# Kernel optimization log

Hardware: AMD Instinct MI355X
Metric: run time of the kernel (lower is better)

Reference implementation:

```python
import jax, jax.numpy as jnp
import numpy as np

NUM_ITEMS = 50000
EMB = 16
SLATE = 10
HID = 512
LAT = 64
RESP = 1024
BATCH = 256


def _linear_params(k, out_dim, in_dim):
    kw, kb = jax.random.split(k)
    s = 1.0 / np.sqrt(in_dim)
    W = jax.random.uniform(kw, (out_dim, in_dim), jnp.float32, -s, s)
    b = jax.random.uniform(kb, (out_dim,), jnp.float32, -s, s)
    return W, b


def setup_inputs() -> dict:
    key = jax.random.key(0)
    ks = jax.random.split(key, 10)
    user_repr = jax.random.randint(ks[0], (BATCH, NUM_ITEMS), 0, 2, dtype=jnp.int32)
    slate = jax.random.randint(ks[1], (BATCH, SLATE), 0, NUM_ITEMS, dtype=jnp.int32)
    response_encoded = jax.random.uniform(ks[2], (BATCH, RESP), jnp.float32)
    eps = jax.random.normal(ks[3], (BATCH, LAT), jnp.float32)
    emb = jax.random.normal(ks[4], (NUM_ITEMS, EMB), jnp.float32)
    in_enc = SLATE * EMB + EMB + RESP
    W_enc, b_enc = _linear_params(ks[5], HID, in_enc)
    W_mu, b_mu = _linear_params(ks[6], LAT, HID)
    W_lv, b_lv = _linear_params(ks[7], LAT, HID)
    in_dec = LAT + EMB + RESP
    W_d1, b_d1 = _linear_params(ks[8], HID, in_dec)
    W_d2, b_d2 = _linear_params(ks[9], SLATE * EMB, HID)
    return {"user_repr": user_repr, "slate": slate, "response_encoded": response_encoded,
            "eps": eps, "emb": emb, "W_enc": W_enc, "b_enc": b_enc,
            "W_mu": W_mu, "b_mu": b_mu, "W_lv": W_lv, "b_lv": b_lv,
            "W_d1": W_d1, "b_d1": b_d1, "W_d2": W_d2, "b_d2": b_d2}


def reference(user_repr, slate, response_encoded, eps, emb,
              W_enc, b_enc, W_mu, b_mu, W_lv, b_lv, W_d1, b_d1, W_d2, b_d2):
    # Ragged embedding-mean pooling over interacted items (vectorized segment mean):
    # mean of emb rows where user_repr==1  ==  (indicator @ emb) / count
    uf = user_repr.astype(jnp.float32)                       # [B, N]
    counts = jnp.sum(uf, axis=1, keepdims=True)              # [B, 1]
    user = (uf @ emb) / counts                               # [B, E]

    cond = jnp.concatenate([user, response_encoded], axis=1)  # [B, E+R]
    slate_emb = emb[slate]                                    # [B, K, E]
    slate_vec = slate_emb.reshape(-1, SLATE * EMB)            # [B, K*E]
    x = jnp.concatenate([slate_vec, cond], axis=1)

    # encoder
    h = jax.nn.relu(x @ W_enc.T + b_enc)
    z_mean = h @ W_mu.T + b_mu
    z_log_var = h @ W_lv.T + b_lv

    # reparameterized sample
    z = z_mean + eps * jnp.exp(0.5 * z_log_var)

    # decoder
    dz = jnp.concatenate([z, cond], axis=1)
    dh = jax.nn.relu(dz @ W_d1.T + b_d1)
    rx = jax.nn.relu(dh @ W_d2.T + b_d2)                      # [B, K*E]
    rx = rx.reshape(-1, SLATE, EMB)                           # [B, K, E]

    # scores vs all items, softmax over items
    logits = jnp.einsum('bkh,nh->bkn', rx, emb)               # [B, K, N]
    probs = jax.nn.softmax(logits, axis=2)
    recon_slate = jnp.argmax(probs, axis=2)                   # [B, K]
    recon_resp = jnp.take_along_axis(probs, slate[:, :, None], axis=2)[..., 0]  # [B, K]
    return z_mean, z_log_var, recon_slate, recon_resp
```

## Files before the change

### kernel.cpp

```cpp
#include <hip/hip_runtime.h>

#define NITEMS 50000
#define EMBD   16
#define NSLATE 10
#define HIDD   512
#define LATD   64
#define RESPD  1024
#define BATCH  256
#define NCHUNK 8
#define CHUNK  6250
#define PCHUNK 3125
#define LOG2E  1.44269504088896340736f
#define SHIFT  64.0f

#define OUT_ZM 0
#define OUT_ZLV 16384
#define OUT_RS 32768
#define OUT_RR 35328

#define WS_X    0
#define WS_DZ   307200
#define WS_P2   0
#define WS_PP   589824
#define WS_PART 589824
#define WS_RX   1114112
#define WS_SPS  1155072
#define WS_SPM  1175552
#define WS_SPA  1196032

__global__ __launch_bounds__(256) void pool_part(const int* __restrict__ u,
    const float* __restrict__ emb, float* __restrict__ pp) {
  int b = blockIdx.x, c = blockIdx.y, t = threadIdx.x;
  float acc[16];
  #pragma unroll
  for (int i = 0; i < 16; ++i) acc[i] = 0.0f;
  float cnt = 0.0f;
  const int* ub = u + (size_t)b * NITEMS;
  int n1 = c * PCHUNK + PCHUNK;
  for (int n = c * PCHUNK + t; n < n1; n += 256) {
    if (ub[n]) {
      const float4* e4 = (const float4*)(emb + (size_t)n * 16);
      float4 a = e4[0], bb = e4[1], cc = e4[2], dd = e4[3];
      acc[0] += a.x;  acc[1] += a.y;  acc[2] += a.z;  acc[3] += a.w;
      acc[4] += bb.x; acc[5] += bb.y; acc[6] += bb.z; acc[7] += bb.w;
      acc[8] += cc.x; acc[9] += cc.y; acc[10] += cc.z; acc[11] += cc.w;
      acc[12] += dd.x; acc[13] += dd.y; acc[14] += dd.z; acc[15] += dd.w;
      cnt += 1.0f;
    }
  }
  #pragma unroll
  for (int off = 32; off > 0; off >>= 1) {
    #pragma unroll
    for (int i = 0; i < 16; ++i) acc[i] += __shfl_down(acc[i], off);
    cnt += __shfl_down(cnt, off);
  }
  int lane = t & 63, wv = t >> 6;
  if (lane == 0) {
    float* dst = pp + ((size_t)(b * 16 + c) * 4 + wv) * 17;
    #pragma unroll
    for (int i = 0; i < 16; ++i) dst[i] = acc[i];
    dst[16] = cnt;
  }
}

__global__ __launch_bounds__(256) void build_x(const float* __restrict__ pp,
    const int* __restrict__ slate, const float* __restrict__ resp,
    const float* __restrict__ emb, float* __restrict__ x, float* __restrict__ dz) {
  __shared__ float fin[17];
  int b = blockIdx.x, t = threadIdx.x;
  if (t < 17) {
    float a = 0.f;
    const float* p = pp + (size_t)b * 64 * 17 + t;
    #pragma unroll
    for (int w = 0; w < 64; ++w) a += p[w * 17];
    fin[t] = a;
  }
  __syncthreads();
  float inv = 1.0f / fin[16];
  if (t < 16) {
    float uv = fin[t] * inv;
    x[b * 1200 + 160 + t] = uv;
    dz[b * 1104 + 64 + t] = uv;
  }
  if (t >= 32 && t < 192) {
    int i = t - 32;
    int k = i >> 4, e = i & 15;
    int it = slate[b * 10 + k];
    x[b * 1200 + i] = emb[(size_t)it * 16 + e];
  }
  for (int i = t; i < 1024; i += 256) {
    float r = resp[b * 1024 + i];
    x[b * 1200 + 176 + i] = r;
    dz[b * 1104 + 80 + i] = r;
  }
}

__global__ __launch_bounds__(256) void gemm64(const float* __restrict__ A,
    const float* __restrict__ B, float* __restrict__ P, int M, int N, int K, int kChunk) {
  __shared__ float As[16][68];
  __shared__ float Bs[16][68];
  int tid = threadIdx.x;
  int m0 = blockIdx.y * 64, n0 = blockIdx.x * 64;
  int ks = blockIdx.z * kChunk;
  int ke = ks + kChunk; if (ke > K) ke = K;
  int sr = tid >> 2;
  int sc = (tid & 3) * 4;
  int tx = tid & 15, ty = tid >> 4;
  float acc[4][4];
  #pragma unroll
  for (int i = 0; i < 4; ++i)
    #pragma unroll
    for (int j = 0; j < 4; ++j) acc[i][j] = 0.f;
  for (int k0 = ks; k0 < ke; k0 += 16) {
    float4 av = make_float4(0.f, 0.f, 0.f, 0.f);
    float4 bv = make_float4(0.f, 0.f, 0.f, 0.f);
    if (k0 + sc < ke)
      av = *(const float4*)(A + (size_t)(m0 + sr) * K + k0 + sc);
    if (k0 + sc < ke && n0 + sr < N)
      bv = *(const float4*)(B + (size_t)(n0 + sr) * K + k0 + sc);
    __syncthreads();
    As[sc][sr] = av.x; As[sc + 1][sr] = av.y; As[sc + 2][sr] = av.z; As[sc + 3][sr] = av.w;
    Bs[sc][sr] = bv.x; Bs[sc + 1][sr] = bv.y; Bs[sc + 2][sr] = bv.z; Bs[sc + 3][sr] = bv.w;
    __syncthreads();
    #pragma unroll
    for (int kk = 0; kk < 16; ++kk) {
      float4 a4 = *(const float4*)&As[kk][4 * ty];
      float4 b4 = *(const float4*)&Bs[kk][4 * tx];
      float a[4] = {a4.x, a4.y, a4.z, a4.w};
      float b[4] = {b4.x, b4.y, b4.z, b4.w};
      #pragma unroll
      for (int i = 0; i < 4; ++i)
        #pragma unroll
        for (int j = 0; j < 4; ++j) acc[i][j] = fmaf(a[i], b[j], acc[i][j]);
    }
  }
  float* Pz = P + (size_t)blockIdx.z * M * N;
  #pragma unroll
  for (int i = 0; i < 4; ++i) {
    int m = m0 + 4 * ty + i, n = n0 + 4 * tx;
    if (n < N)
      *(float4*)(Pz + (size_t)m * N + n) = make_float4(acc[i][0], acc[i][1], acc[i][2], acc[i][3]);
  }
}

__global__ __launch_bounds__(128) void mulv_z_kernel(const float* __restrict__ part,
    const float* __restrict__ benc,
    const float* __restrict__ Wmu, const float* __restrict__ bmu,
    const float* __restrict__ Wlv, const float* __restrict__ blv,
    const float* __restrict__ eps, float* __restrict__ out, float* __restrict__ dz) {
  __shared__ __align__(16) float hs[512];
  __shared__ float zms[64], zlvs[64];
  int b = blockIdx.x, t = threadIdx.x;
  for (int i = t; i < 512; i += 128) {
    float a = benc[i];
    #pragma unroll
    for (int s = 0; s < 4; ++s) a += part[(size_t)s * 131072 + b * 512 + i];
    hs[i] = fmaxf(a, 0.f);
  }
  __syncthreads();
  const float* Wr = (t < 64) ? (Wmu + (size_t)t * 512) : (Wlv + (size_t)(t - 64) * 512);
  float bias = (t < 64) ? bmu[t] : blv[t - 64];
  const float4* w4 = (const float4*)Wr;
  const float4* h4 = (const float4*)hs;
  float a0 = 0.f, a1 = 0.f, a2 = 0.f, a3 = 0.f;
  #pragma unroll 4
  for (int i = 0; i < 128; ++i) {
    float4 w = w4[i], hv = h4[i];
    a0 = fmaf(w.x, hv.x, a0); a1 = fmaf(w.y, hv.y, a1);
    a2 = fmaf(w.z, hv.z, a2); a3 = fmaf(w.w, hv.w, a3);
  }
  float acc = (a0 + a1) + (a2 + a3) + bias;
  if (t < 64) { out[OUT_ZM + b * 64 + t] = acc; zms[t] = acc; }
  else        { out[OUT_ZLV + b * 64 + (t - 64)] = acc; zlvs[t - 64] = acc; }
  __syncthreads();
  if (t < 64) {
    float zv = fmaf(eps[b * 64 + t], __builtin_amdgcn_exp2f(0.7213475204444817f * zlvs[t]), zms[t]);
    dz[b * 1104 + t] = zv;
  }
}

__global__ __launch_bounds__(256) void gemm_d2(const float* __restrict__ part,
    const float* __restrict__ bd1, const float* __restrict__ W, float* __restrict__ p2) {
  __shared__ float As[16][68];
  __shared__ float Bs[16][68];
  const int N = 160;
  int tid = threadIdx.x;
  int m0 = blockIdx.y * 64, n0 = blockIdx.x * 64;
  int ks = blockIdx.z * 64, ke = ks + 64;
  int sr = tid >> 2, sc = (tid & 3) * 4;
  int tx = tid & 15, ty = tid >> 4;
  float acc[4][4];
  #pragma unroll
  for (int i = 0; i < 4; ++i)
    #pragma unroll
    for (int j = 0; j < 4; ++j) acc[i][j] = 0.f;
  for (int k0 = ks; k0 < ke; k0 += 16) {
    int col = k0 + sc;
    const float* p = part + (size_t)(m0 + sr) * 512 + col;
    float4 a0 = *(const float4*)(p);
    float4 a1 = *(const float4*)(p + 131072);
    float4 a2 = *(const float4*)(p + 262144);
    float4 a3 = *(const float4*)(p + 393216);
    float4 bb = *(const float4*)(bd1 + col);
    float4 av;
    av.x = fmaxf(a0.x + a1.x + a2.x + a3.x + bb.x, 0.f);
    av.y = fmaxf(a0.y + a1.y + a2.y + a3.y + bb.y, 0.f);
    av.z = fmaxf(a0.z + a1.z + a2.z + a3.z + bb.z, 0.f);
    av.w = fmaxf(a0.w + a1.w + a2.w + a3.w + bb.w, 0.f);
    float4 bv = make_float4(0.f, 0.f, 0.f, 0.f);
    if (n0 + sr < N)
      bv = *(const float4*)(W + (size_t)(n0 + sr) * 512 + col);
    __syncthreads();
    As[sc][sr] = av.x; As[sc + 1][sr] = av.y; As[sc + 2][sr] = av.z; As[sc + 3][sr] = av.w;
    Bs[sc][sr] = bv.x; Bs[sc + 1][sr] = bv.y; Bs[sc + 2][sr] = bv.z; Bs[sc + 3][sr] = bv.w;
    __syncthreads();
    #pragma unroll
    for (int kk = 0; kk < 16; ++kk) {
      float4 a4 = *(const float4*)&As[kk][4 * ty];
      float4 b4 = *(const float4*)&Bs[kk][4 * tx];
      float a[4] = {a4.x, a4.y, a4.z, a4.w};
      float b[4] = {b4.x, b4.y, b4.z, b4.w};
      #pragma unroll
      for (int i = 0; i < 4; ++i)
        #pragma unroll
        for (int j = 0; j < 4; ++j) acc[i][j] = fmaf(a[i], b[j], acc[i][j]);
    }
  }
  float* Pz = p2 + (size_t)blockIdx.z * 40960;
  #pragma unroll
  for (int i = 0; i < 4; ++i) {
    int m = m0 + 4 * ty + i, n = n0 + 4 * tx;
    if (n < N)
      *(float4*)(Pz + (size_t)m * 160 + n) = make_float4(acc[i][0], acc[i][1], acc[i][2], acc[i][3]);
  }
}

__global__ __launch_bounds__(256, 2) void score_part(const float* __restrict__ p2,
    const float* __restrict__ bd2, const float* __restrict__ emb,
    float* __restrict__ rx, float* __restrict__ psg, float* __restrict__ pmg,
    int* __restrict__ pag) {
  __shared__ __align__(16) float rxs[160];
  __shared__ float wm[4][10], wsum[4][10];
  __shared__ int wa[4][10];
  int b = blockIdx.x, c = blockIdx.y, t = threadIdx.x;
  if (t < 160) {
    float a = bd2[t];
    #pragma unroll
    for (int z = 0; z < 8; ++z) a += p2[(size_t)z * 40960 + b * 160 + t];
    float v = fmaxf(a, 0.f) * LOG2E;
    rxs[t] = v;
    if (c == 0) rx[b * 160 + t] = v;
  }
  __syncthreads();
  float m[10], s[10];
  int am[10];
  #pragma unroll
  for (int k = 0; k < 10; ++k) { m[k] = -3.402823466e38f; s[k] = 0.f; am[k] = 0; }
  int nBase = c * CHUNK;
  const float4* ep = (const float4*)emb;
  #pragma unroll 1
  for (int j = 0; j < 12; ++j) {
    int n0 = nBase + j * 512 + t;
    float4 e[2][4];
    #pragma unroll
    for (int it = 0; it < 2; ++it) {
      const float4* p = ep + (size_t)(n0 + it * 256) * 4;
      e[it][0] = p[0]; e[it][1] = p[1]; e[it][2] = p[2]; e[it][3] = p[3];
    }
    #pragma unroll
    for (int k = 0; k < 10; ++k) {
      float4 r0 = *(const float4*)(rxs + k * 16);
      float4 r1 = *(const float4*)(rxs + k * 16 + 4);
      float4 r2 = *(const float4*)(rxs + k * 16 + 8);
      float4 r3 = *(const float4*)(rxs + k * 16 + 12);
      #pragma unroll
      for (int it = 0; it < 2; ++it) {
        float x0 = fmaf(e[it][0].x, r0.x, -SHIFT);
        float x1 = e[it][1].x * r1.x;
        float x2 = e[it][2].x * r2.x;
        float x3 = e[it][3].x * r3.x;
        x0 = fmaf(e[it][0].y, r0.y, x0);
        x1 = fmaf(e[it][1].y, r1.y, x1);
        x2 = fmaf(e[it][2].y, r2.y, x2);
        x3 = fmaf(e[it][3].y, r3.y, x3);
        x0 = fmaf(e[it][0].z, r0.z, x0);
        x1 = fmaf(e[it][1].z, r1.z, x1);
        x2 = fmaf(e[it][2].z, r2.z, x2);
        x3 = fmaf(e[it][3].z, r3.z, x3);
        x0 = fmaf(e[it][0].w, r0.w, x0);
        x1 = fmaf(e[it][1].w, r1.w, x1);
        x2 = fmaf(e[it][2].w, r2.w, x2);
        x3 = fmaf(e[it][3].w, r3.w, x3);
        float x = (x0 + x1) + (x2 + x3);
        s[k] += __builtin_amdgcn_exp2f(x);
        if (x > m[k]) { m[k] = x; am[k] = n0 + it * 256; }
      }
    }
  }
  if (t < CHUNK - 6144) {
    int n = nBase + 6144 + t;
    const float4* p = ep + (size_t)n * 4;
    float4 e0 = p[0], e1 = p[1], e2 = p[2], e3 = p[3];
    #pragma unroll
    for (int k = 0; k < 10; ++k) {
      const float4 r0 = *(const float4*)(rxs + k * 16);
      const float4 r1 = *(const float4*)(rxs + k * 16 + 4);
      const float4 r2 = *(const float4*)(rxs + k * 16 + 8);
      const float4 r3 = *(const float4*)(rxs + k * 16 + 12);
      float x0 = fmaf(e0.w, r0.w, fmaf(e0.z, r0.z, fmaf(e0.y, r0.y, fmaf(e0.x, r0.x, -SHIFT))));
      float x1 = fmaf(e1.w, r1.w, fmaf(e1.z, r1.z, fmaf(e1.y, r1.y, e1.x * r1.x)));
      float x2 = fmaf(e2.w, r2.w, fmaf(e2.z, r2.z, fmaf(e2.y, r2.y, e2.x * r2.x)));
      float x3 = fmaf(e3.w, r3.w, fmaf(e3.z, r3.z, fmaf(e3.y, r3.y, e3.x * r3.x)));
      float x = (x0 + x1) + (x2 + x3);
      s[k] += __builtin_amdgcn_exp2f(x);
      if (x > m[k]) { m[k] = x; am[k] = n; }
    }
  }
  #pragma unroll
  for (int off = 32; off > 0; off >>= 1) {
    #pragma unroll
    for (int k = 0; k < 10; ++k) {
      s[k] += __shfl_down(s[k], off);
      float om = __shfl_down(m[k], off);
      int oa = __shfl_down(am[k], off);
      bool take = (om > m[k]) || (om == m[k] && oa < am[k]);
      am[k] = take ? oa : am[k];
      m[k] = fmaxf(m[k], om);
    }
  }
  int lane = t & 63, wv = t >> 6;
  if (lane == 0) {
    #pragma unroll
    for (int k = 0; k < 10; ++k) { wm[wv][k] = m[k]; wsum[wv][k] = s[k]; wa[wv][k] = am[k]; }
  }
  __syncthreads();
  if (t < 10) {
    int k = t;
    float M = wm[0][k], S = wsum[0][k];
    int AM = wa[0][k];
    #pragma unroll
    for (int w = 1; w < 4; ++w) {
      float m2 = wm[w][k];
      int oa = wa[w][k];
      bool take = (m2 > M) || (m2 == M && oa < AM);
      AM = take ? oa : AM;
      M = fmaxf(M, m2);
      S += wsum[w][k];
    }
    int idx = (b * NCHUNK + c) * 10 + k;
    psg[idx] = S; pmg[idx] = M; pag[idx] = AM;
  }
}

__global__ __launch_bounds__(256) void score_final(const float* __restrict__ psg,
    const float* __restrict__ pmg, const int* __restrict__ pag,
    const float* __restrict__ rx, const float* __restrict__ emb,
    const int* __restrict__ slate, float* __restrict__ out) {
  int tid = blockIdx.x * 256 + threadIdx.x;
  if (tid >= BATCH * 10) return;
  int b = tid / 10, k = tid % 10;
  int base = b * NCHUNK * 10 + k;
  float S = 0.f, M = -3.402823466e38f;
  int AM = 2147483647;
  #pragma unroll
  for (int c = 0; c < NCHUNK; ++c) {
    S += psg[base + c * 10];
    float m2 = pmg[base + c * 10];
    int oa = pag[base + c * 10];
    bool take = (m2 > M) || (m2 == M && oa < AM);
    AM = take ? oa : AM;
    M = fmaxf(M, m2);
  }
  int it = slate[b * 10 + k];
  const float* er = emb + (size_t)it * 16;
  const float* rr = rx + b * 160 + k * 16;
  float xs = -SHIFT;
  #pragma unroll
  for (int e = 0; e < 16; ++e) xs = fmaf(rr[e], er[e], xs);
  out[OUT_RS + b * 10 + k] = (float)AM;
  out[OUT_RR + b * 10 + k] = __builtin_amdgcn_exp2f(xs) / S;
}

extern "C" void kernel_launch(void* const* d_in, const int* in_sizes, int n_in,
                              void* d_out, int out_size, void* d_ws, size_t ws_size,
                              hipStream_t stream) {
  const int* user_repr = (const int*)d_in[0];
  const int* slate = (const int*)d_in[1];
  const float* resp = (const float*)d_in[2];
  const float* eps = (const float*)d_in[3];
  const float* emb = (const float*)d_in[4];
  const float* W_enc = (const float*)d_in[5];
  const float* b_enc = (const float*)d_in[6];
  const float* W_mu = (const float*)d_in[7];
  const float* b_mu = (const float*)d_in[8];
  const float* W_lv = (const float*)d_in[9];
  const float* b_lv = (const float*)d_in[10];
  const float* W_d1 = (const float*)d_in[11];
  const float* b_d1 = (const float*)d_in[12];
  const float* W_d2 = (const float*)d_in[13];
  const float* b_d2 = (const float*)d_in[14];
  float* out = (float*)d_out;
  float* ws = (float*)d_ws;

  float* x    = ws + WS_X;
  float* dz   = ws + WS_DZ;
  float* p2   = ws + WS_P2;
  float* pp   = ws + WS_PP;
  float* part = ws + WS_PART;
  float* rx   = ws + WS_RX;
  float* sps  = ws + WS_SPS;
  float* spm  = ws + WS_SPM;
  int*   spa  = (int*)(ws + WS_SPA);

  pool_part<<<dim3(256, 16), 256, 0, stream>>>(user_repr, emb, pp);
  build_x<<<256, 256, 0, stream>>>(pp, slate, resp, emb, x, dz);
  gemm64<<<dim3(8, 4, 4), 256, 0, stream>>>(x, W_enc, part, 256, 512, 1200, 300);
  mulv_z_kernel<<<256, 128, 0, stream>>>(part, b_enc, W_mu, b_mu, W_lv, b_lv, eps, out, dz);
  gemm64<<<dim3(8, 4, 4), 256, 0, stream>>>(dz, W_d1, part, 256, 512, 1104, 276);
  gemm_d2<<<dim3(3, 4, 8), 256, 0, stream>>>(part, b_d1, W_d2, p2);
  score_part<<<dim3(256, 8), 256, 0, stream>>>(p2, b_d2, emb, rx, sps, spm, spa);
  score_final<<<10, 256, 0, stream>>>(sps, spm, spa, rx, emb, slate, out);
}
```

Measured before the change: 325.6 us.

## Compute item scores with split-bf16 MFMA instead of scalar FP32 FMAs

Replaces the scalar FP32 scoring of all 50000 items against each batch's 10 reconstructed vectors with 32x32x16 bf16 MFMA tiles. To keep near-FP32 accuracy, both the item embeddings and the rx vectors are split into three bf16 parts, and six cross-term MFMAs are accumulated. A new rx_prep kernel precomputes the split rx fragments. Work is repartitioned so each wave handles 32 slate columns over a range of item tiles, which produces 64 partial reductions per column that score_final merges. This trades VALU FMA work for matrix-core work plus per-tile bf16 splitting, at some risk to argmax tie behaviour and precision.

```diff
diff --git a/kernel.cpp b/kernel.cpp
--- a/kernel.cpp
+++ b/kernel.cpp
@@ -7,11 +7,14 @@
 #define LATD   64
 #define RESPD  1024
 #define BATCH  256
-#define NCHUNK 8
-#define CHUNK  6250
 #define PCHUNK 3125
 #define LOG2E  1.44269504088896340736f
 #define SHIFT  64.0f
+
+#define NCOL   2560
+#define NT     1563
+#define IC     64
+#define TPC    25
 
 #define OUT_ZM 0
 #define OUT_ZLV 16384
@@ -23,10 +26,28 @@
 #define WS_P2   0
 #define WS_PP   589824
 #define WS_PART 589824
+#define WS_PS   589824
+#define WS_PM   753664
+#define WS_PA   917504
 #define WS_RX   1114112
-#define WS_SPS  1155072
-#define WS_SPM  1175552
-#define WS_SPA  1196032
+#define WS_RXS0 1155072
+#define WS_RXS1 1175552
+#define WS_RXS2 1196032
+
+typedef __attribute__((ext_vector_type(8))) short bfrag;
+typedef __attribute__((ext_vector_type(16))) float f32x16;
+
+__device__ __forceinline__ float bfround(float v) {
+  unsigned u = __float_as_uint(v);
+  unsigned r = (u + 0x7FFFu + ((u >> 16) & 1u)) & 0xFFFF0000u;
+  return __uint_as_float(r);
+}
+__device__ __forceinline__ float bftrunc(float v) {
+  return __uint_as_float(__float_as_uint(v) & 0xFFFF0000u);
+}
+__device__ __forceinline__ short bf16bits(float v) {
+  return (short)(__float_as_uint(v) >> 16);
+}
 
 __global__ __launch_bounds__(256) void pool_part(const int* __restrict__ u,
     const float* __restrict__ emb, float* __restrict__ pp) {
@@ -235,120 +256,97 @@
   }
 }
 
-__global__ __launch_bounds__(256, 2) void score_part(const float* __restrict__ p2,
-    const float* __restrict__ bd2, const float* __restrict__ emb,
-    float* __restrict__ rx, float* __restrict__ psg, float* __restrict__ pmg,
-    int* __restrict__ pag) {
-  __shared__ __align__(16) float rxs[160];
-  __shared__ float wm[4][10], wsum[4][10];
-  __shared__ int wa[4][10];
-  int b = blockIdx.x, c = blockIdx.y, t = threadIdx.x;
-  if (t < 160) {
-    float a = bd2[t];
-    #pragma unroll
-    for (int z = 0; z < 8; ++z) a += p2[(size_t)z * 40960 + b * 160 + t];
-    float v = fmaxf(a, 0.f) * LOG2E;
-    rxs[t] = v;
-    if (c == 0) rx[b * 160 + t] = v;
-  }
-  __syncthreads();
-  float m[10], s[10];
-  int am[10];
-  #pragma unroll
-  for (int k = 0; k < 10; ++k) { m[k] = -3.402823466e38f; s[k] = 0.f; am[k] = 0; }
-  int nBase = c * CHUNK;
-  const float4* ep = (const float4*)emb;
+__global__ __launch_bounds__(256) void rx_prep(const float* __restrict__ p2,
+    const float* __restrict__ bd2, float* __restrict__ rx,
+    unsigned short* __restrict__ rx0, unsigned short* __restrict__ rx1,
+    unsigned short* __restrict__ rx2) {
+  int b = blockIdx.x, t = threadIdx.x;
+  if (t >= 160) return;
+  float a = bd2[t];
+  #pragma unroll
+  for (int z = 0; z < 8; ++z) a += p2[(size_t)z * 40960 + b * 160 + t];
+  float v = fmaxf(a, 0.f) * LOG2E;
+  rx[b * 160 + t] = v;
+  int col = b * 10 + (t >> 4), e = t & 15;
+  float f0 = bfround(v);
+  float d1 = v - f0;
+  float f1 = bfround(d1);
+  float d2 = d1 - f1;
+  float f2 = bfround(d2);
+  rx0[col * 16 + e] = (unsigned short)(__float_as_uint(f0) >> 16);
+  rx1[col * 16 + e] = (unsigned short)(__float_as_uint(f1) >> 16);
+  rx2[col * 16 + e] = (unsigned short)(__float_as_uint(f2) >> 16);
+}
+
+__global__ __launch_bounds__(256) void score_mfma(const float* __restrict__ emb,
+    const unsigned short* __restrict__ rx0, const unsigned short* __restrict__ rx1,
+    const unsigned short* __restrict__ rx2,
+    float* __restrict__ ps, float* __restrict__ pm, int* __restrict__ pa) {
+  int t = threadIdx.x;
+  int w = t >> 6, l = t & 63;
+  int ln = l & 31, hf = l >> 5;
+  int cg = blockIdx.x * 4 + w;
+  int ic = blockIdx.y;
+  int col = cg * 32 + ln;
+  size_t boff = (size_t)col * 16 + hf * 8;
+  bfrag b0 = *(const bfrag*)(rx0 + boff);
+  bfrag b1 = *(const bfrag*)(rx1 + boff);
+  bfrag b2 = *(const bfrag*)(rx2 + boff);
+  float s_acc = 0.f, mmax = -3.402823466e38f;
+  int am = 0x7FFFFFFF;
+  int ts = ic * TPC, te = ts + TPC;
+  if (te > NT) te = NT;
   #pragma unroll 1
-  for (int j = 0; j < 12; ++j) {
-    int n0 = nBase + j * 512 + t;
-    float4 e[2][4];
-    #pragma unroll
-    for (int it = 0; it < 2; ++it) {
-      const float4* p = ep + (size_t)(n0 + it * 256) * 4;
-      e[it][0] = p[0]; e[it][1] = p[1]; e[it][2] = p[2]; e[it][3] = p[3];
-    }
-    #pragma unroll
-    for (int k = 0; k < 10; ++k) {
-      float4 r0 = *(const float4*)(rxs + k * 16);
-      float4 r1 = *(const float4*)(rxs + k * 16 + 4);
-      float4 r2 = *(const float4*)(rxs + k * 16 + 8);
-      float4 r3 = *(const float4*)(rxs + k * 16 + 12);
+  for (int tile = ts; tile < te; ++tile) {
+    int r = tile * 32 + ln;
+    float4 e0, e1;
+    if (r < NITEMS) {
+      const float4* p = (const float4*)(emb + (size_t)r * 16 + hf * 8);
+      e0 = p[0]; e1 = p[1];
+    } else {
+      e0 = make_float4(-128.f, -128.f, -128.f, -128.f);
+      e1 = e0;
+    }
+    float ev[8] = {e0.x, e0.y, e0.z, e0.w, e1.x, e1.y, e1.z, e1.w};
+    bfrag a0, a1, a2;
+    #pragma unroll
+    for (int i = 0; i < 8; ++i) {
+      float v = ev[i];
+      float f0 = bfround(v);
+      float d1 = v - f0;
+      float f1 = bftrunc(d1);
+      float d2 = d1 - f1;
+      a0[i] = bf16bits(f0);
+      a1[i] = bf16bits(f1);
+      a2[i] = bf16bits(d2);
+    }
+    f32x16 acc;
+    #pragma unroll
+    for (int i = 0; i < 16; ++i) acc[i] = -SHIFT;
+    acc = __builtin_amdgcn_mfma_f32_32x32x16_bf16(a1, b1, acc, 0, 0, 0);
+    acc = __builtin_amdgcn_mfma_f32_32x32x16_bf16(a2, b0, acc, 0, 0, 0);
+    acc = __builtin_amdgcn_mfma_f32_32x32x16_bf16(a0, b2, acc, 0, 0, 0);
+    acc = __builtin_amdgcn_mfma_f32_32x32x16_bf16(a1, b0, acc, 0, 0, 0);
+    acc = __builtin_amdgcn_mfma_f32_32x32x16_bf16(a0, b1, acc, 0, 0, 0);
+    acc = __builtin_amdgcn_mfma_f32_32x32x16_bf16(a0, b0, acc, 0, 0, 0);
+    int base = tile * 32 + 4 * hf;
+    #pragma unroll
+    for (int g = 0; g < 4; ++g) {
       #pragma unroll
-      for (int it = 0; it < 2; ++it) {
-        float x0 = fmaf(e[it][0].x, r0.x, -SHIFT);
-        float x1 = e[it][1].x * r1.x;
-        float x2 = e[it][2].x * r2.x;
-        float x3 = e[it][3].x * r3.x;
-        x0 = fmaf(e[it][0].y, r0.y, x0);
-        x1 = fmaf(e[it][1].y, r1.y, x1);
-        x2 = fmaf(e[it][2].y, r2.y, x2);
-        x3 = fmaf(e[it][3].y, r3.y, x3);
-        x0 = fmaf(e[it][0].z, r0.z, x0);
-        x1 = fmaf(e[it][1].z, r1.z, x1);
-        x2 = fmaf(e[it][2].z, r2.z, x2);
-        x3 = fmaf(e[it][3].z, r3.z, x3);
-        x0 = fmaf(e[it][0].w, r0.w, x0);
-        x1 = fmaf(e[it][1].w, r1.w, x1);
-        x2 = fmaf(e[it][2].w, r2.w, x2);
-        x3 = fmaf(e[it][3].w, r3.w, x3);
-        float x = (x0 + x1) + (x2 + x3);
-        s[k] += __builtin_amdgcn_exp2f(x);
-        if (x > m[k]) { m[k] = x; am[k] = n0 + it * 256; }
+      for (int q = 0; q < 4; ++q) {
+        float x = acc[g * 4 + q];
+        s_acc += __builtin_amdgcn_exp2f(x);
+        if (x > mmax) { mmax = x; am = base + 8 * g + q; }
       }
     }
   }
-  if (t < CHUNK - 6144) {
-    int n = nBase + 6144 + t;
-    const float4* p = ep + (size_t)n * 4;
-    float4 e0 = p[0], e1 = p[1], e2 = p[2], e3 = p[3];
-    #pragma unroll
-    for (int k = 0; k < 10; ++k) {
-      const float4 r0 = *(const float4*)(rxs + k * 16);
-      const float4 r1 = *(const float4*)(rxs + k * 16 + 4);
-      const float4 r2 = *(const float4*)(rxs + k * 16 + 8);
-      const float4 r3 = *(const float4*)(rxs + k * 16 + 12);
-      float x0 = fmaf(e0.w, r0.w, fmaf(e0.z, r0.z, fmaf(e0.y, r0.y, fmaf(e0.x, r0.x, -SHIFT))));
-      float x1 = fmaf(e1.w, r1.w, fmaf(e1.z, r1.z, fmaf(e1.y, r1.y, e1.x * r1.x)));
-      float x2 = fmaf(e2.w, r2.w, fmaf(e2.z, r2.z, fmaf(e2.y, r2.y, e2.x * r2.x)));
-      float x3 = fmaf(e3.w, r3.w, fmaf(e3.z, r3.z, fmaf(e3.y, r3.y, e3.x * r3.x)));
-      float x = (x0 + x1) + (x2 + x3);
-      s[k] += __builtin_amdgcn_exp2f(x);
-      if (x > m[k]) { m[k] = x; am[k] = n; }
-    }
-  }
-  #pragma unroll
-  for (int off = 32; off > 0; off >>= 1) {
-    #pragma unroll
-    for (int k = 0; k < 10; ++k) {
-      s[k] += __shfl_down(s[k], off);
-      float om = __shfl_down(m[k], off);
-      int oa = __shfl_down(am[k], off);
-      bool take = (om > m[k]) || (om == m[k] && oa < am[k]);
-      am[k] = take ? oa : am[k];
-      m[k] = fmaxf(m[k], om);
-    }
-  }
-  int lane = t & 63, wv = t >> 6;
-  if (lane == 0) {
-    #pragma unroll
-    for (int k = 0; k < 10; ++k) { wm[wv][k] = m[k]; wsum[wv][k] = s[k]; wa[wv][k] = am[k]; }
-  }
-  __syncthreads();
-  if (t < 10) {
-    int k = t;
-    float M = wm[0][k], S = wsum[0][k];
-    int AM = wa[0][k];
-    #pragma unroll
-    for (int w = 1; w < 4; ++w) {
-      float m2 = wm[w][k];
-      int oa = wa[w][k];
-      bool take = (m2 > M) || (m2 == M && oa < AM);
-      AM = take ? oa : AM;
-      M = fmaxf(M, m2);
-      S += wsum[w][k];
-    }
-    int idx = (b * NCHUNK + c) * 10 + k;
-    psg[idx] = S; pmg[idx] = M; pag[idx] = AM;
+  s_acc += __shfl_xor(s_acc, 32);
+  float om = __shfl_xor(mmax, 32);
+  int oa = __shfl_xor(am, 32);
+  if (om > mmax || (om == mmax && oa < am)) { mmax = om; am = oa; }
+  if (hf == 0) {
+    int idx = ic * NCOL + col;
+    ps[idx] = s_acc; pm[idx] = mmax; pa[idx] = am;
   }
 }
 
@@ -359,14 +357,13 @@
   int tid = blockIdx.x * 256 + threadIdx.x;
   if (tid >= BATCH * 10) return;
   int b = tid / 10, k = tid % 10;
-  int base = b * NCHUNK * 10 + k;
   float S = 0.f, M = -3.402823466e38f;
   int AM = 2147483647;
-  #pragma unroll
-  for (int c = 0; c < NCHUNK; ++c) {
-    S += psg[base + c * 10];
-    float m2 = pmg[base + c * 10];
-    int oa = pag[base + c * 10];
+  for (int c = 0; c < IC; ++c) {
+    int idx = c * NCOL + tid;
+    S += psg[idx];
+    float m2 = pmg[idx];
+    int oa = pag[idx];
     bool take = (m2 > M) || (m2 == M && oa < AM);
     AM = take ? oa : AM;
     M = fmaxf(M, m2);
@@ -407,10 +404,13 @@
   float* p2   = ws + WS_P2;
   float* pp   = ws + WS_PP;
   float* part = ws + WS_PART;
+  float* ps   = ws + WS_PS;
+  float* pmb  = ws + WS_PM;
+  int*   pab  = (int*)(ws + WS_PA);
   float* rx   = ws + WS_RX;
-  float* sps  = ws + WS_SPS;
-  float* spm  = ws + WS_SPM;
-  int*   spa  = (int*)(ws + WS_SPA);
+  unsigned short* rx0 = (unsigned short*)(ws + WS_RXS0);
+  unsigned short* rx1 = (unsigned short*)(ws + WS_RXS1);
+  unsigned short* rx2 = (unsigned short*)(ws + WS_RXS2);
 
   pool_part<<<dim3(256, 16), 256, 0, stream>>>(user_repr, emb, pp);
   build_x<<<256, 256, 0, stream>>>(pp, slate, resp, emb, x, dz);
@@ -418,6 +418,7 @@
   mulv_z_kernel<<<256, 128, 0, stream>>>(part, b_enc, W_mu, b_mu, W_lv, b_lv, eps, out, dz);
   gemm64<<<dim3(8, 4, 4), 256, 0, stream>>>(dz, W_d1, part, 256, 512, 1104, 276);
   gemm_d2<<<dim3(3, 4, 8), 256, 0, stream>>>(part, b_d1, W_d2, p2);
-  score_part<<<dim3(256, 8), 256, 0, stream>>>(p2, b_d2, emb, rx, sps, spm, spa);
-  score_final<<<10, 256, 0, stream>>>(sps, spm, spa, rx, emb, slate, out);
-}
+  rx_prep<<<256, 256, 0, stream>>>(p2, b_d2, rx, rx0, rx1, rx2);
+  score_mfma<<<dim3(20, IC), 256, 0, stream>>>(emb, rx0, rx1, rx2, ps, pmb, pab);
+  score_final<<<10, 256, 0, stream>>>(ps, pmb, pab, rx, emb, slate, out);
+}
```

New measurement: 286.7 us. 1.14x faster.
